# Kernel optimization log

Measured on AMD Instinct MI355X. Metric: run time of the kernel, lower is better.

Reference implementation:

```python
import jax, jax.numpy as jnp
import numpy as np

P = 3            # spline degree per axis (cubic)
NC = 64          # control points per axis
DOUT = 3         # output dimension of control points
NQ = 1_000_000   # number of query points


def open_uniform_knots(n, p):
    interior = np.linspace(0.0, 1.0, n - p + 1)
    return np.concatenate([np.zeros(p), interior, np.ones(p)]).astype(np.float32)  # len n+p+1


def bspline_basis(t, p, x):
    """Cox-de Boor basis. t:[n+p+1], x:[N] -> (i:[N,p+1] int, b:[N,p+1] float)."""
    n_basis = t.shape[0] - p - 1
    t_clamped = jnp.clip(x, t[p], t[-p - 1])
    k = jnp.searchsorted(t, t_clamped, side='right') - 1
    k = jnp.clip(k, p, n_basis - 1)                       # [N]
    i = k[:, None] + jnp.arange(-p, 1)                    # [N, p+1] global basis idx
    d = jnp.broadcast_to(jnp.eye(p + 1, dtype=x.dtype), (x.shape[0], p + 1, p + 1))
    for r in range(1, p + 1):
        j = jnp.arange(p, r - 1, -1)                      # [p-r+1]
        jk = j[None, :] + k[:, None]                      # [N, p-r+1]
        left = t[jk - p]
        right = t[jk + 1 - r]
        alpha = ((x[:, None] - left) / (right - left))[..., None]  # [N, p-r+1, 1]
        d = d.at[:, j].set((1.0 - alpha) * d[:, j - 1] + alpha * d[:, j])
    return i, d[:, p]                                     # basis values sum to 1


def setup_inputs() -> dict:
    key = jax.random.key(0)
    kq, kc = jax.random.split(key)
    queries = jax.random.uniform(kq, (NQ, 3), dtype=jnp.float32)
    control_points = jax.random.normal(kc, (NC * NC * NC, DOUT), dtype=jnp.float32)
    t = jnp.asarray(open_uniform_knots(NC, P))
    return {"queries": queries, "control_points": control_points,
            "tx": t, "ty": t, "tz": t}


def reference(queries, control_points, tx, ty, tz):
    px = py = pz = P
    ix, bx = bspline_basis(tx, px, queries[:, 0])   # [N,px+1]
    iy, by = bspline_basis(ty, py, queries[:, 1])
    iz, bz = bspline_basis(tz, pz, queries[:, 2])
    nx = tx.shape[0] - px - 1
    ny = ty.shape[0] - py - 1
    # flat index into [nx*ny*nz] control grid: ix + nx*(iy + ny*iz)
    flat_idx = (ix[:, :, None, None]
                + nx * (iy[:, None, :, None] + ny * iz[:, None, None, :]))  # [N,px+1,py+1,pz+1]
    cp_sel = control_points[flat_idx]                   # [N,px+1,py+1,pz+1,DOUT]
    y = jnp.einsum('na,nb,nc,nabcd->nd', bx, by, bz, cp_sel)
    return y
```

## Files before the change

kernel.cpp:

```cpp
#include <hip/hip_runtime.h>


#define NC 64
#define NSEG 61
#define NCELLS 512
#define WDIM 11
#define CAP 2560
#define CHUNK 1024
#define NCHUNK 3
#define NITEMS (NCELLS * NCHUNK)
#define EVAL_BLOCKS 1024
#define CHUNK_S 2048
#define OVF_CAP 4096

typedef float vfloat4 __attribute__((ext_vector_type(4)));

__device__ __forceinline__ float rcpf(float x) {
#if __has_builtin(__builtin_amdgcn_rcpf)
  return __builtin_amdgcn_rcpf(x);
#else
  return 1.0f / x;
#endif
}

__device__ __forceinline__ int span_of(float x) {
  float xc = fminf(fmaxf(x, 0.0f), 1.0f);
  int j = (int)floorf(xc * (float)NSEG);
  return j > NSEG - 1 ? NSEG - 1 : (j < 0 ? 0 : j);
}

__device__ __forceinline__ float knotv(int i) {
  float v = (float)(i - 3) * (1.0f / (float)NSEG);
  return fminf(fmaxf(v, 0.0f), 1.0f);
}

__device__ __forceinline__ void basis4(float x, int j, float N[4]) {
  float xc = fminf(fmaxf(x, 0.0f), 1.0f);
  int k = j + 3;
  float left[4], right[4];
  N[0] = 1.0f;
#pragma unroll
  for (int jj = 1; jj <= 3; ++jj) {
    left[jj] = xc - knotv(k + 1 - jj);
    right[jj] = knotv(k + jj) - xc;
    float saved = 0.0f;
#pragma unroll
    for (int r = 0; r < jj; ++r) {
      float temp = N[r] * rcpf(right[r + 1] + left[jj - r]);
      N[r] = saved + right[r + 1] * temp;
      saved = left[jj - r] * temp;
    }
    N[jj] = saved;
  }
}

__device__ __forceinline__ void eval_point(float x, float y, float z, int jx,
                                           int jy, int jz,
                                           const float* __restrict__ cp,
                                           float o[3]) {
  float Nx[4], Ny[4], Nz[4];
  basis4(x, jx, Nx);
  basis4(y, jy, Ny);
  basis4(z, jz, Nz);
  float ax = 0, ay = 0, az = 0;
#pragma unroll 1
  for (int c = 0; c < 4; ++c) {
#pragma unroll
    for (int b = 0; b < 4; ++b) {
      float w = Ny[b] * Nz[c];
      const float* row = cp + 3 * (size_t)(jx + NC * (jy + b + NC * (jz + c)));
      vfloat4 f0, f1, f2;
      __builtin_memcpy(&f0, row + 0, 16);
      __builtin_memcpy(&f1, row + 4, 16);
      __builtin_memcpy(&f2, row + 8, 16);
      ax += w * (Nx[0] * f0.x + Nx[1] * f0.w + Nx[2] * f1.z + Nx[3] * f2.y);
      ay += w * (Nx[0] * f0.y + Nx[1] * f1.x + Nx[2] * f1.w + Nx[3] * f2.z);
      az += w * (Nx[0] * f0.z + Nx[1] * f1.y + Nx[2] * f2.x + Nx[3] * f2.w);
    }
  }
  o[0] = ax; o[1] = ay; o[2] = az;
}

__device__ __forceinline__ void scan512_excl(int* arr) {
  int tid = threadIdx.x;
  int c = arr[tid];
#pragma unroll
  for (int off = 1; off < 512; off <<= 1) {
    int t = (tid >= off) ? arr[tid - off] : 0;
    __syncthreads();
    arr[tid] += t;
    __syncthreads();
  }
  arr[tid] -= c;
  __syncthreads();
}


__global__ __launch_bounds__(512) void scatter_capped(
    const float* __restrict__ q, int* __restrict__ gcursor,
    int* __restrict__ ovfcnt, float4* __restrict__ ovf,
    float4* __restrict__ sorted, int nq) {
  __shared__ int hist[NCELLS];
  __shared__ int gb[NCELLS];
  __shared__ int lcur[NCELLS];
  __shared__ float4 stage[CHUNK_S];
  __shared__ int addr[CHUNK_S];
  int b = blockIdx.x, tid = threadIdx.x;
  hist[tid] = 0;
  lcur[tid] = 0;
  __syncthreads();

  int s = b * CHUNK_S, e = min(nq, s + CHUNK_S);
  int nblk = e - s;
  float xs[4], ys[4], zs[4];
  int cells[4];
  unsigned us[4];
#pragma unroll
  for (int it = 0; it < 4; ++it) {
    int i = s + it * 512 + tid;
    cells[it] = -1;
    if (i < e) {
      float xyz[3];
      __builtin_memcpy(xyz, q + 3 * (size_t)i, 12);
      xs[it] = xyz[0]; ys[it] = xyz[1]; zs[it] = xyz[2];
      int jx = span_of(xyz[0]), jy = span_of(xyz[1]), jz = span_of(xyz[2]);
      cells[it] = (jx >> 3) + 8 * (jy >> 3) + 64 * (jz >> 3);
      us[it] = (unsigned)i | ((unsigned)(jx & 7) << 20) |
               ((unsigned)(jy & 7) << 23) | ((unsigned)(jz & 7) << 26);
      atomicAdd(&hist[cells[it]], 1);
    }
  }
  __syncthreads();
  int n0 = hist[tid];
  gb[tid] = n0 ? atomicAdd(&gcursor[tid], n0) : 0;
  __syncthreads();
  scan512_excl(hist);
#pragma unroll
  for (int it = 0; it < 4; ++it) {
    int cell = cells[it];
    if (cell < 0) continue;
    int rank = atomicAdd(&lcur[cell], 1);
    int rloc = hist[cell] + rank;
    int rg = gb[cell] + rank;
    if (rg < CAP) {
      stage[rloc] = make_float4(xs[it], ys[it], zs[it],
                                __int_as_float((int)us[it]));
      addr[rloc] = cell * CAP + rg;
    } else {
      addr[rloc] = -1;
      int p = atomicAdd(ovfcnt, 1);
      if (p < OVF_CAP)
        ovf[p] = make_float4(xs[it], ys[it], zs[it],
                             __int_as_float((int)(us[it] & 0xFFFFFu)));
    }
  }
  __syncthreads();
  for (int j = tid; j < nblk; j += 512) {
    int a = addr[j];
    if (a >= 0) sorted[a] = stage[j];
  }
}


__global__ __launch_bounds__(512) void eval_kernel(
    const float4* __restrict__ sorted, const int* __restrict__ cellcnt,
    const float* __restrict__ cp, float* __restrict__ out,
    int* __restrict__ qhead) {
  __shared__ float4 lds[WDIM * WDIM * WDIM];
  __shared__ int bins[NCELLS];
  __shared__ unsigned short order[CHUNK];
  __shared__ int s_item;
  int tid = threadIdx.x;

  for (;;) {
    __syncthreads();
    if (tid == 0) s_item = atomicAdd(qhead, 1);
    __syncthreads();
    int item = s_item;
    if (item >= NITEMS) break;
    int chunkid = item >> 9;
    int cid = item & (NCELLS - 1);
    int cnt = min(cellcnt[cid], CAP);
    int q0 = chunkid * CHUNK;
    if (q0 >= cnt) continue;
    int n = min(cnt - q0, CHUNK);
    size_t base = (size_t)cid * CAP + q0;
    int ox = (cid & 7) * 8, oy = ((cid >> 3) & 7) * 8, oz = (cid >> 6) * 8;

    for (int e2 = tid; e2 < WDIM * WDIM * WDIM; e2 += 512) {
      int lx = e2 % WDIM, t = e2 / WDIM;
      int ly = t % WDIM, lz = t / WDIM;
      int gx = min(ox + lx, NC - 1), gy = min(oy + ly, NC - 1),
          gz = min(oz + lz, NC - 1);
      const float* p = cp + 3 * (size_t)(gx + NC * (gy + NC * gz));
      lds[e2] = make_float4(p[0], p[1], p[2], 0.0f);
    }
    bins[tid] = 0;
    int k0 = -1, k1 = -1, r0 = 0, r1 = 0;
    if (tid < n)
      k0 = (int)(((unsigned)__float_as_int(sorted[base + tid].w) >> 20) & 511u);
    if (tid + 512 < n)
      k1 = (int)(((unsigned)__float_as_int(sorted[base + tid + 512].w) >> 20) &
                 511u);
    __syncthreads();
    if (k0 >= 0) r0 = atomicAdd(&bins[k0], 1);
    if (k1 >= 0) r1 = atomicAdd(&bins[k1], 1);
    __syncthreads();
    scan512_excl(bins);
    if (k0 >= 0) order[bins[k0] + r0] = (unsigned short)tid;
    if (k1 >= 0) order[bins[k1] + r1] = (unsigned short)(tid + 512);
    __syncthreads();

    for (int t2 = tid; t2 < n; t2 += 512) {
      int lidx = order[t2];
      float4 s = sorted[base + lidx];
      unsigned u = (unsigned)__float_as_int(s.w);
      int oi = (int)(u & 0xFFFFFu);
      int lx0 = (int)((u >> 20) & 7), ly0 = (int)((u >> 23) & 7),
          lz0 = (int)((u >> 26) & 7);
      float Nx[4], Ny[4], Nz[4];
      basis4(s.x, ox + lx0, Nx);
      basis4(s.y, oy + ly0, Ny);
      basis4(s.z, oz + lz0, Nz);

      float ax = 0.0f, ay = 0.0f, az = 0.0f;
#pragma unroll
      for (int c = 0; c < 4; ++c) {
#pragma unroll
        for (int b = 0; b < 4; ++b) {
          float w = Ny[b] * Nz[c];
          const float4* row = &lds[((lz0 + c) * WDIM + (ly0 + b)) * WDIM + lx0];
          float4 p0 = row[0], p1 = row[1], p2 = row[2], p3 = row[3];
          ax += w * (Nx[0] * p0.x + Nx[1] * p1.x + Nx[2] * p2.x + Nx[3] * p3.x);
          ay += w * (Nx[0] * p0.y + Nx[1] * p1.y + Nx[2] * p2.y + Nx[3] * p3.y);
          az += w * (Nx[0] * p0.z + Nx[1] * p1.z + Nx[2] * p2.z + Nx[3] * p3.z);
        }
      }
      float o[3] = {ax, ay, az};
      __builtin_memcpy(out + 3 * (size_t)oi, o, 12);
    }
  }
}

__global__ __launch_bounds__(256) void ovf_kernel(const float4* __restrict__ ovf,
                                                  const int* __restrict__ ovfcnt,
                                                  const float* __restrict__ cp,
                                                  float* __restrict__ out) {
  int n = min(*ovfcnt, OVF_CAP);
  for (int i = blockIdx.x * 256 + threadIdx.x; i < n; i += gridDim.x * 256) {
    float4 s = ovf[i];
    int oi = __float_as_int(s.w);
    float o[3];
    eval_point(s.x, s.y, s.z, span_of(s.x), span_of(s.y), span_of(s.z), cp, o);
    __builtin_memcpy(out + 3 * (size_t)oi, o, 12);
  }
}

__global__ __launch_bounds__(256) void spline_direct_kernel(
    const float* __restrict__ q, const float* __restrict__ cp,
    float* __restrict__ out, int nq) {
  int i = blockIdx.x * 256 + threadIdx.x;
  if (i >= nq) return;
  float xyz[3];
  __builtin_memcpy(xyz, q + 3 * (size_t)i, 12);
  float o[3];
  eval_point(xyz[0], xyz[1], xyz[2], span_of(xyz[0]), span_of(xyz[1]),
             span_of(xyz[2]), cp, o);
  __builtin_memcpy(out + 3 * (size_t)i, o, 12);
}

extern "C" void kernel_launch(void* const* d_in, const int* in_sizes, int n_in,
                              void* d_out, int out_size, void* d_ws,
                              size_t ws_size, hipStream_t stream) {
  const float* queries = (const float*)d_in[0];
  const float* control = (const float*)d_in[1];
  float* out = (float*)d_out;
  int nq = in_sizes[0] / 3;

  size_t meta = (NCELLS + 2) * sizeof(int);
  size_t metap = (meta + 15) & ~15ull;
  size_t need = metap + (size_t)OVF_CAP * 16 + (size_t)NCELLS * CAP * 16;

  if (nq <= (1 << 20) && ws_size >= need) {
    int* gcursor = (int*)d_ws;
    int* ovfcnt = gcursor + NCELLS;
    int* qhead = gcursor + NCELLS + 1;
    float4* ovf = (float4*)((char*)d_ws + metap);
    float4* sorted = ovf + OVF_CAP;
    hipMemsetAsync(d_ws, 0, meta, stream);
    int nb = (nq + CHUNK_S - 1) / CHUNK_S;
    scatter_capped<<<nb, 512, 0, stream>>>(queries, gcursor, ovfcnt, ovf,
                                           sorted, nq);
    eval_kernel<<<EVAL_BLOCKS, 512, 0, stream>>>(sorted, gcursor, control, out,
                                                 qhead);
    ovf_kernel<<<4, 256, 0, stream>>>(ovf, ovfcnt, control, out);
  } else {
    spline_direct_kernel<<<(nq + 255) / 256, 256, 0, stream>>>(queries, control,
                                                               out, nq);
  }
}
```

Before: 134.8 us.

## Scatter directly without LDS staging, wave-shuffle scans, and fold overflow into eval

The scatter kernel now writes each point straight to its global bucket slot using the rank returned by the LDS histogram atomic, which drops the LDS staging buffer, the block scan and the second pass. Block scans use wavefront shuffles instead of a Hillis-Steele loop with many barriers. Eval chunks shrink to one point per thread, and the overflow pass moves into the eval kernel so one launch disappears. In exchange, global writes from scatter are no longer coalesced, and the smaller chunks mean more work items and more control-point window loads per cell.

```diff
diff --git a/kernel.cpp b/kernel.cpp
--- a/kernel.cpp
+++ b/kernel.cpp
@@ -6,11 +6,11 @@
 #define NCELLS 512
 #define WDIM 11
 #define CAP 2560
-#define CHUNK 1024
-#define NCHUNK 3
+#define CHUNK 512
+#define NCHUNK 5
 #define NITEMS (NCELLS * NCHUNK)
 #define EVAL_BLOCKS 1024
-#define CHUNK_S 2048
+#define CHUNK_S 1024
 #define OVF_CAP 4096
 
 typedef float vfloat4 __attribute__((ext_vector_type(4)));
@@ -81,42 +81,50 @@
   o[0] = ax; o[1] = ay; o[2] = az;
 }
 
-__device__ __forceinline__ void scan512_excl(int* arr) {
+__device__ __forceinline__ void scan512_excl(int* arr, int* aux) {
   int tid = threadIdx.x;
-  int c = arr[tid];
-#pragma unroll
-  for (int off = 1; off < 512; off <<= 1) {
-    int t = (tid >= off) ? arr[tid - off] : 0;
-    __syncthreads();
-    arr[tid] += t;
-    __syncthreads();
-  }
-  arr[tid] -= c;
-  __syncthreads();
-}
-
-
-__global__ __launch_bounds__(512) void scatter_capped(
+  int lane = tid & 63, wv = tid >> 6;
+  int v = arr[tid];
+  int inc = v;
+#pragma unroll
+  for (int off = 1; off < 64; off <<= 1) {
+    int t = __shfl_up(inc, off, 64);
+    if (lane >= off) inc += t;
+  }
+  if (lane == 63) aux[wv] = inc;
+  __syncthreads();
+  if (tid < 64) {
+    int a = (tid < 8) ? aux[tid] : 0;
+    int ainc = a;
+#pragma unroll
+    for (int off = 1; off < 8; off <<= 1) {
+      int t = __shfl_up(ainc, off, 64);
+      if (lane >= off) ainc += t;
+    }
+    if (tid < 8) aux[tid] = ainc - a;
+  }
+  __syncthreads();
+  arr[tid] = (inc - v) + aux[wv];
+  __syncthreads();
+}
+
+
+__global__ __launch_bounds__(512) void scatter_direct(
     const float* __restrict__ q, int* __restrict__ gcursor,
     int* __restrict__ ovfcnt, float4* __restrict__ ovf,
     float4* __restrict__ sorted, int nq) {
   __shared__ int hist[NCELLS];
   __shared__ int gb[NCELLS];
-  __shared__ int lcur[NCELLS];
-  __shared__ float4 stage[CHUNK_S];
-  __shared__ int addr[CHUNK_S];
-  int b = blockIdx.x, tid = threadIdx.x;
+  int tid = threadIdx.x;
+  int s = blockIdx.x * CHUNK_S, e = min(nq, s + CHUNK_S);
   hist[tid] = 0;
-  lcur[tid] = 0;
-  __syncthreads();
-
-  int s = b * CHUNK_S, e = min(nq, s + CHUNK_S);
-  int nblk = e - s;
-  float xs[4], ys[4], zs[4];
-  int cells[4];
-  unsigned us[4];
-#pragma unroll
-  for (int it = 0; it < 4; ++it) {
+  __syncthreads();
+
+  float xs[2], ys[2], zs[2];
+  int cells[2], rank[2];
+  unsigned us[2];
+#pragma unroll
+  for (int it = 0; it < 2; ++it) {
     int i = s + it * 512 + tid;
     cells[it] = -1;
     if (i < e) {
@@ -127,37 +135,29 @@
       cells[it] = (jx >> 3) + 8 * (jy >> 3) + 64 * (jz >> 3);
       us[it] = (unsigned)i | ((unsigned)(jx & 7) << 20) |
                ((unsigned)(jy & 7) << 23) | ((unsigned)(jz & 7) << 26);
-      atomicAdd(&hist[cells[it]], 1);
+      rank[it] = atomicAdd(&hist[cells[it]], 1);
     }
   }
   __syncthreads();
   int n0 = hist[tid];
   gb[tid] = n0 ? atomicAdd(&gcursor[tid], n0) : 0;
   __syncthreads();
-  scan512_excl(hist);
-#pragma unroll
-  for (int it = 0; it < 4; ++it) {
+#pragma unroll
+  for (int it = 0; it < 2; ++it) {
     int cell = cells[it];
     if (cell < 0) continue;
-    int rank = atomicAdd(&lcur[cell], 1);
-    int rloc = hist[cell] + rank;
-    int rg = gb[cell] + rank;
+    int rg = gb[cell] + rank[it];
+    float4 v = make_float4(xs[it], ys[it], zs[it],
+                           __int_as_float((int)us[it]));
     if (rg < CAP) {
-      stage[rloc] = make_float4(xs[it], ys[it], zs[it],
-                                __int_as_float((int)us[it]));
-      addr[rloc] = cell * CAP + rg;
+      sorted[cell * CAP + rg] = v;
     } else {
-      addr[rloc] = -1;
       int p = atomicAdd(ovfcnt, 1);
-      if (p < OVF_CAP)
-        ovf[p] = make_float4(xs[it], ys[it], zs[it],
-                             __int_as_float((int)(us[it] & 0xFFFFFu)));
-    }
-  }
-  __syncthreads();
-  for (int j = tid; j < nblk; j += 512) {
-    int a = addr[j];
-    if (a >= 0) sorted[a] = stage[j];
+      if (p < OVF_CAP) {
+        v.w = __int_as_float((int)(us[it] & 0xFFFFFu));
+        ovf[p] = v;
+      }
+    }
   }
 }
 
@@ -165,10 +165,12 @@
 __global__ __launch_bounds__(512) void eval_kernel(
     const float4* __restrict__ sorted, const int* __restrict__ cellcnt,
     const float* __restrict__ cp, float* __restrict__ out,
-    int* __restrict__ qhead) {
+    int* __restrict__ qhead, const int* __restrict__ ovfcnt,
+    const float4* __restrict__ ovf) {
   __shared__ float4 lds[WDIM * WDIM * WDIM];
   __shared__ int bins[NCELLS];
   __shared__ unsigned short order[CHUNK];
+  __shared__ int aux[8];
   __shared__ int s_item;
   int tid = threadIdx.x;
 
@@ -196,23 +198,20 @@
       lds[e2] = make_float4(p[0], p[1], p[2], 0.0f);
     }
     bins[tid] = 0;
-    int k0 = -1, k1 = -1, r0 = 0, r1 = 0;
-    if (tid < n)
-      k0 = (int)(((unsigned)__float_as_int(sorted[base + tid].w) >> 20) & 511u);
-    if (tid + 512 < n)
-      k1 = (int)(((unsigned)__float_as_int(sorted[base + tid + 512].w) >> 20) &
-                 511u);
+    int k0 = -1, r0 = 0;
+    if (tid < n) {
+      const float* wp = (const float*)(sorted + base + tid);
+      k0 = (int)(((unsigned)__float_as_int(wp[3]) >> 20) & 511u);
+    }
     __syncthreads();
     if (k0 >= 0) r0 = atomicAdd(&bins[k0], 1);
-    if (k1 >= 0) r1 = atomicAdd(&bins[k1], 1);
-    __syncthreads();
-    scan512_excl(bins);
+    __syncthreads();
+    scan512_excl(bins, aux);
     if (k0 >= 0) order[bins[k0] + r0] = (unsigned short)tid;
-    if (k1 >= 0) order[bins[k1] + r1] = (unsigned short)(tid + 512);
-    __syncthreads();
-
-    for (int t2 = tid; t2 < n; t2 += 512) {
-      int lidx = order[t2];
+    __syncthreads();
+
+    if (tid < n) {
+      int lidx = order[tid];
       float4 s = sorted[base + lidx];
       unsigned u = (unsigned)__float_as_int(s.w);
       int oi = (int)(u & 0xFFFFFu);
@@ -240,14 +239,9 @@
       __builtin_memcpy(out + 3 * (size_t)oi, o, 12);
     }
   }
-}
-
-__global__ __launch_bounds__(256) void ovf_kernel(const float4* __restrict__ ovf,
-                                                  const int* __restrict__ ovfcnt,
-                                                  const float* __restrict__ cp,
-                                                  float* __restrict__ out) {
-  int n = min(*ovfcnt, OVF_CAP);
-  for (int i = blockIdx.x * 256 + threadIdx.x; i < n; i += gridDim.x * 256) {
+
+  int novf = min(*ovfcnt, OVF_CAP);
+  for (int i = blockIdx.x * 512 + tid; i < novf; i += EVAL_BLOCKS * 512) {
     float4 s = ovf[i];
     int oi = __float_as_int(s.w);
     float o[3];
@@ -289,11 +283,10 @@
     float4* sorted = ovf + OVF_CAP;
     hipMemsetAsync(d_ws, 0, meta, stream);
     int nb = (nq + CHUNK_S - 1) / CHUNK_S;
-    scatter_capped<<<nb, 512, 0, stream>>>(queries, gcursor, ovfcnt, ovf,
+    scatter_direct<<<nb, 512, 0, stream>>>(queries, gcursor, ovfcnt, ovf,
                                            sorted, nq);
     eval_kernel<<<EVAL_BLOCKS, 512, 0, stream>>>(sorted, gcursor, control, out,
-                                                 qhead);
-    ovf_kernel<<<4, 256, 0, stream>>>(ovf, ovfcnt, control, out);
+                                                 qhead, ovfcnt, ovf);
   } else {
     spline_direct_kernel<<<(nq + 255) / 256, 256, 0, stream>>>(queries, control,
                                                                out, nq);
```

Result: slower. 159.1 us (+18.0%).

## Use wave-shuffle scan, static per-cell half partitions, fold overflow into eval

Applied to the files above, without the earlier changes.

Replaces the barrier-heavy Hillis-Steele LDS scan with a wavefront shuffle scan plus a small cross-wave pass, cutting the number of __syncthreads. The eval kernel drops the atomic work queue and instead assigns each cell to two blocks that each take half its points (up to 1280). The separate overflow kernel launch is merged into the tail of the eval kernel. The trade-off is that static partitioning loses dynamic load balancing, and each block now stages the control-point window for its half-cell.

```diff
diff --git a/kernel.cpp b/kernel.cpp
--- a/kernel.cpp
+++ b/kernel.cpp
@@ -6,10 +6,8 @@
 #define NCELLS 512
 #define WDIM 11
 #define CAP 2560
-#define CHUNK 1024
-#define NCHUNK 3
-#define NITEMS (NCELLS * NCHUNK)
-#define EVAL_BLOCKS 1024
+#define PARTMAX 1280
+#define EVAL_BLOCKS (2 * NCELLS)
 #define CHUNK_S 2048
 #define OVF_CAP 4096
 
@@ -81,37 +79,51 @@
   o[0] = ax; o[1] = ay; o[2] = az;
 }
 
-__device__ __forceinline__ void scan512_excl(int* arr) {
+__device__ __forceinline__ void scan512_excl(int* arr, int* aux) {
   int tid = threadIdx.x;
-  int c = arr[tid];
-#pragma unroll
-  for (int off = 1; off < 512; off <<= 1) {
-    int t = (tid >= off) ? arr[tid - off] : 0;
-    __syncthreads();
-    arr[tid] += t;
-    __syncthreads();
-  }
-  arr[tid] -= c;
-  __syncthreads();
-}
-
-
-__global__ __launch_bounds__(512) void scatter_capped(
+  int lane = tid & 63, wv = tid >> 6;
+  int v = arr[tid];
+  int inc = v;
+#pragma unroll
+  for (int off = 1; off < 64; off <<= 1) {
+    int t = __shfl_up(inc, off, 64);
+    if (lane >= off) inc += t;
+  }
+  if (lane == 63) aux[wv] = inc;
+  __syncthreads();
+  if (tid < 64) {
+    int a = (tid < 8) ? aux[tid] : 0;
+    int ainc = a;
+#pragma unroll
+    for (int off = 1; off < 8; off <<= 1) {
+      int t = __shfl_up(ainc, off, 64);
+      if (lane >= off) ainc += t;
+    }
+    if (tid < 8) aux[tid] = ainc - a;
+  }
+  __syncthreads();
+  arr[tid] = (inc - v) + aux[wv];
+  __syncthreads();
+}
+
+
+__global__ __launch_bounds__(512) void scatter_staged(
     const float* __restrict__ q, int* __restrict__ gcursor,
     int* __restrict__ ovfcnt, float4* __restrict__ ovf,
     float4* __restrict__ sorted, int nq) {
   __shared__ int hist[NCELLS];
   __shared__ int gb[NCELLS];
   __shared__ int lcur[NCELLS];
+  __shared__ int aux[8];
   __shared__ float4 stage[CHUNK_S];
   __shared__ int addr[CHUNK_S];
-  int b = blockIdx.x, tid = threadIdx.x;
+  int tid = threadIdx.x;
+  int s = blockIdx.x * CHUNK_S, e = min(nq, s + CHUNK_S);
+  int nblk = e - s;
   hist[tid] = 0;
   lcur[tid] = 0;
   __syncthreads();
 
-  int s = b * CHUNK_S, e = min(nq, s + CHUNK_S);
-  int nblk = e - s;
   float xs[4], ys[4], zs[4];
   int cells[4];
   unsigned us[4];
@@ -133,8 +145,7 @@
   __syncthreads();
   int n0 = hist[tid];
   gb[tid] = n0 ? atomicAdd(&gcursor[tid], n0) : 0;
-  __syncthreads();
-  scan512_excl(hist);
+  scan512_excl(hist, aux);
 #pragma unroll
   for (int it = 0; it < 4; ++it) {
     int cell = cells[it];
@@ -165,25 +176,19 @@
 __global__ __launch_bounds__(512) void eval_kernel(
     const float4* __restrict__ sorted, const int* __restrict__ cellcnt,
     const float* __restrict__ cp, float* __restrict__ out,
-    int* __restrict__ qhead) {
+    const int* __restrict__ ovfcnt, const float4* __restrict__ ovf) {
   __shared__ float4 lds[WDIM * WDIM * WDIM];
   __shared__ int bins[NCELLS];
-  __shared__ unsigned short order[CHUNK];
-  __shared__ int s_item;
+  __shared__ unsigned short order[PARTMAX];
+  __shared__ int aux[8];
   int tid = threadIdx.x;
-
-  for (;;) {
-    __syncthreads();
-    if (tid == 0) s_item = atomicAdd(qhead, 1);
-    __syncthreads();
-    int item = s_item;
-    if (item >= NITEMS) break;
-    int chunkid = item >> 9;
-    int cid = item & (NCELLS - 1);
-    int cnt = min(cellcnt[cid], CAP);
-    int q0 = chunkid * CHUNK;
-    if (q0 >= cnt) continue;
-    int n = min(cnt - q0, CHUNK);
+  int cid = blockIdx.x >> 1, part = blockIdx.x & 1;
+  int cnt = min(cellcnt[cid], CAP);
+  int h = cnt >> 1;
+  int q0 = part ? h : 0;
+  int n = part ? (cnt - h) : h;
+
+  if (n > 0) {
     size_t base = (size_t)cid * CAP + q0;
     int ox = (cid & 7) * 8, oy = ((cid >> 3) & 7) * 8, oz = (cid >> 6) * 8;
 
@@ -196,32 +201,40 @@
       lds[e2] = make_float4(p[0], p[1], p[2], 0.0f);
     }
     bins[tid] = 0;
-    int k0 = -1, k1 = -1, r0 = 0, r1 = 0;
+    int k0 = -1, k1 = -1, k2 = -1, r0 = 0, r1 = 0, r2 = 0;
     if (tid < n)
-      k0 = (int)(((unsigned)__float_as_int(sorted[base + tid].w) >> 20) & 511u);
+      k0 = (int)(((unsigned)__float_as_int(
+                     ((const float*)(sorted + base + tid))[3]) >> 20) & 511u);
     if (tid + 512 < n)
-      k1 = (int)(((unsigned)__float_as_int(sorted[base + tid + 512].w) >> 20) &
+      k1 = (int)(((unsigned)__float_as_int(
+                     ((const float*)(sorted + base + tid + 512))[3]) >> 20) &
+                 511u);
+    if (tid + 1024 < n)
+      k2 = (int)(((unsigned)__float_as_int(
+                     ((const float*)(sorted + base + tid + 1024))[3]) >> 20) &
                  511u);
     __syncthreads();
     if (k0 >= 0) r0 = atomicAdd(&bins[k0], 1);
     if (k1 >= 0) r1 = atomicAdd(&bins[k1], 1);
+    if (k2 >= 0) r2 = atomicAdd(&bins[k2], 1);
     __syncthreads();
-    scan512_excl(bins);
+    scan512_excl(bins, aux);
     if (k0 >= 0) order[bins[k0] + r0] = (unsigned short)tid;
     if (k1 >= 0) order[bins[k1] + r1] = (unsigned short)(tid + 512);
+    if (k2 >= 0) order[bins[k2] + r2] = (unsigned short)(tid + 1024);
     __syncthreads();
 
     for (int t2 = tid; t2 < n; t2 += 512) {
       int lidx = order[t2];
-      float4 s = sorted[base + lidx];
-      unsigned u = (unsigned)__float_as_int(s.w);
+      float4 sp = sorted[base + lidx];
+      unsigned u = (unsigned)__float_as_int(sp.w);
       int oi = (int)(u & 0xFFFFFu);
       int lx0 = (int)((u >> 20) & 7), ly0 = (int)((u >> 23) & 7),
           lz0 = (int)((u >> 26) & 7);
       float Nx[4], Ny[4], Nz[4];
-      basis4(s.x, ox + lx0, Nx);
-      basis4(s.y, oy + ly0, Ny);
-      basis4(s.z, oz + lz0, Nz);
+      basis4(sp.x, ox + lx0, Nx);
+      basis4(sp.y, oy + ly0, Ny);
+      basis4(sp.z, oz + lz0, Nz);
 
       float ax = 0.0f, ay = 0.0f, az = 0.0f;
 #pragma unroll
@@ -240,18 +253,14 @@
       __builtin_memcpy(out + 3 * (size_t)oi, o, 12);
     }
   }
-}
-
-__global__ __launch_bounds__(256) void ovf_kernel(const float4* __restrict__ ovf,
-                                                  const int* __restrict__ ovfcnt,
-                                                  const float* __restrict__ cp,
-                                                  float* __restrict__ out) {
-  int n = min(*ovfcnt, OVF_CAP);
-  for (int i = blockIdx.x * 256 + threadIdx.x; i < n; i += gridDim.x * 256) {
-    float4 s = ovf[i];
-    int oi = __float_as_int(s.w);
+
+  int novf = min(*ovfcnt, OVF_CAP);
+  for (int i = blockIdx.x * 512 + tid; i < novf; i += EVAL_BLOCKS * 512) {
+    float4 sp = ovf[i];
+    int oi = __float_as_int(sp.w);
     float o[3];
-    eval_point(s.x, s.y, s.z, span_of(s.x), span_of(s.y), span_of(s.z), cp, o);
+    eval_point(sp.x, sp.y, sp.z, span_of(sp.x), span_of(sp.y), span_of(sp.z),
+               cp, o);
     __builtin_memcpy(out + 3 * (size_t)oi, o, 12);
   }
 }
@@ -277,23 +286,21 @@
   float* out = (float*)d_out;
   int nq = in_sizes[0] / 3;
 
-  size_t meta = (NCELLS + 2) * sizeof(int);
+  size_t meta = (NCELLS + 1) * sizeof(int);
   size_t metap = (meta + 15) & ~15ull;
   size_t need = metap + (size_t)OVF_CAP * 16 + (size_t)NCELLS * CAP * 16;
 
   if (nq <= (1 << 20) && ws_size >= need) {
     int* gcursor = (int*)d_ws;
     int* ovfcnt = gcursor + NCELLS;
-    int* qhead = gcursor + NCELLS + 1;
     float4* ovf = (float4*)((char*)d_ws + metap);
     float4* sorted = ovf + OVF_CAP;
     hipMemsetAsync(d_ws, 0, meta, stream);
     int nb = (nq + CHUNK_S - 1) / CHUNK_S;
-    scatter_capped<<<nb, 512, 0, stream>>>(queries, gcursor, ovfcnt, ovf,
+    scatter_staged<<<nb, 512, 0, stream>>>(queries, gcursor, ovfcnt, ovf,
                                            sorted, nq);
     eval_kernel<<<EVAL_BLOCKS, 512, 0, stream>>>(sorted, gcursor, control, out,
-                                                 qhead);
-    ovf_kernel<<<4, 256, 0, stream>>>(ovf, ovfcnt, control, out);
+                                                 ovfcnt, ovf);
   } else {
     spline_direct_kernel<<<(nq + 255) / 256, 256, 0, stream>>>(queries, control,
                                                                out, nq);
```

Result: no change. 133.2 us (-1.2%).
